# Kernel optimization log

Measured on AMD Instinct MI355X. Metric: run time of the kernel, lower is better.

## Reference

```python
import jax, jax.numpy as jnp
import numpy as np

B, C, H, W = 4, 96, 64, 64
D_STATE, D_CONV, EXPAND = 16, 4, 2
D_INNER = EXPAND * C          # 192
DT_RANK = (C + 15) // 16      # 6
BN_EPS = 1e-5


def setup_inputs() -> dict:
    key = jax.random.key(0)
    ks = jax.random.split(key, 10)
    s = 0.02
    return {
        "x": jax.random.normal(ks[0], (B, C, H, W), jnp.float32),
        # Mamba block params (mamba_ssm layout, no bias on in/out proj)
        "in_proj_w": jax.random.normal(ks[1], (2 * D_INNER, C), jnp.float32) * s,
        "conv1d_w": jax.random.normal(ks[2], (D_INNER, 1, D_CONV), jnp.float32) * s,  # depthwise
        "conv1d_b": jnp.zeros((D_INNER,), jnp.float32),
        "x_proj_w": jax.random.normal(ks[3], (DT_RANK + 2 * D_STATE, D_INNER), jnp.float32) * s,
        "dt_proj_w": jax.random.normal(ks[4], (D_INNER, DT_RANK), jnp.float32) * s,
        "dt_proj_b": jax.random.normal(ks[5], (D_INNER,), jnp.float32) * s,
        "A_log": jnp.log(jnp.tile(jnp.arange(1, D_STATE + 1, dtype=jnp.float32), (D_INNER, 1))),
        "D": jnp.ones((D_INNER,), jnp.float32),
        "out_proj_w": jax.random.normal(ks[6], (C, D_INNER), jnp.float32) * s,
        # trailing ConvBNReLU6 params
        "conv2d_w": jax.random.normal(ks[7], (C, C, 3, 3), jnp.float32) * s,
        "bn_gamma": jnp.ones((C,), jnp.float32),
        "bn_beta": jnp.zeros((C,), jnp.float32),
        "bn_mean": jnp.zeros((C,), jnp.float32),
        "bn_var": jnp.ones((C,), jnp.float32),
    }


def _forward(x, in_proj_w, conv1d_w, conv1d_b, x_proj_w, dt_proj_w, dt_proj_b,
             A_log, D, out_proj_w, conv2d_w, bn_gamma, bn_beta, bn_mean, bn_var):
    b, c, h, w = x.shape
    L = h * w
    seq = x.reshape(b, c, L).transpose(0, 2, 1)              # [B, L, C] tokens
    xz = seq @ in_proj_w.T                                    # [B, L, 2*D_INNER]
    xi, z = jnp.split(xz, 2, axis=-1)

    # depthwise causal conv1d + SiLU
    xi_c = jax.lax.conv_general_dilated(
        xi.transpose(0, 2, 1), conv1d_w, (1,), [(D_CONV - 1, 0)],
        dimension_numbers=("NCH", "OIH", "NCH"), feature_group_count=D_INNER)
    xi = jax.nn.silu((xi_c + conv1d_b[None, :, None]).transpose(0, 2, 1))  # [B, L, D_INNER]

    # input-dependent dt, B, C
    x_dbl = xi @ x_proj_w.T                                   # [B, L, DT_RANK + 2*D_STATE]
    dt, Bm, Cm = jnp.split(x_dbl, [DT_RANK, DT_RANK + D_STATE], axis=-1)
    dt = jax.nn.softplus(dt @ dt_proj_w.T + dt_proj_b)        # [B, L, D_INNER]

    # discretize: dA = exp(dt*A), dBx = dt*B*x
    A = -jnp.exp(A_log)                                       # [D_INNER, D_STATE]
    dA = jnp.exp(dt[..., None] * A)                           # [B, L, D_INNER, D_STATE]
    dBx = dt[..., None] * Bm[:, :, None, :] * xi[..., None]   # [B, L, D_INNER, D_STATE]

    def step(hst, inputs):
        dA_t, dBx_t, C_t = inputs
        hst = dA_t * hst + dBx_t                              # [B, D_INNER, D_STATE]
        y_t = jnp.einsum("bds,bs->bd", hst, C_t)
        return hst, y_t

    h0 = jnp.zeros((b, D_INNER, D_STATE), xi.dtype)
    _, ys = jax.lax.scan(step, h0,
                         (dA.transpose(1, 0, 2, 3), dBx.transpose(1, 0, 2, 3), Cm.transpose(1, 0, 2)))
    y = ys.transpose(1, 0, 2)                                 # [B, L, D_INNER]
    y = (y + xi * D) * jax.nn.silu(z)                         # skip D + gate
    out = y @ out_proj_w.T                                    # [B, L, C]
    xm = out.transpose(0, 2, 1).reshape(b, c, h, w)

    # ConvBNReLU: 3x3 conv (pad 1, no bias) -> BN (inference) -> ReLU6
    xo = jax.lax.conv_general_dilated(xm, conv2d_w, (1, 1), [(1, 1), (1, 1)],
                                      dimension_numbers=("NCHW", "OIHW", "NCHW"))
    inv = bn_gamma / jnp.sqrt(bn_var + BN_EPS)
    xo = xo * inv[None, :, None, None] + (bn_beta - bn_mean * inv)[None, :, None, None]
    return jnp.clip(xo, 0.0, 6.0)


def reference(x, in_proj_w, conv1d_w, conv1d_b, x_proj_w, dt_proj_w, dt_proj_b,
              A_log, D, out_proj_w, conv2d_w, bn_gamma, bn_beta, bn_mean, bn_var):
    return _forward(x, in_proj_w, conv1d_w, conv1d_b, x_proj_w, dt_proj_w, dt_proj_b,
                    A_log, D, out_proj_w, conv2d_w, bn_gamma, bn_beta, bn_mean, bn_var)
```

## Files before the change

### kernel.cpp

```cpp
#include <hip/hip_runtime.h>
#include <math.h>

#define LQ 4096
#define DI 192
#define DS 16
#define NCHUNK 64

__device__ __forceinline__ float siluf_(float v) { return v / (1.f + __expf(-v)); }
__device__ __forceinline__ float softplusf_(float v) { return v > 20.f ? v : log1pf(__expf(v)); }

template <int CTRL>
__device__ __forceinline__ float dpp_add16_(float x) {
    int y = __builtin_amdgcn_update_dpp(0, __float_as_int(x), CTRL, 0xf, 0xf, true);
    return x + __int_as_float(y);
}
template <int CTRL>
__device__ __forceinline__ float dpp_shift_(float x) {
    int y = __builtin_amdgcn_update_dpp(0, __float_as_int(x), CTRL, 0xf, 0xf, true);
    return __int_as_float(y);
}
__device__ __forceinline__ void async_g2l16_(const float* g, float* l) {
    __builtin_amdgcn_global_load_lds(
        (const __attribute__((address_space(1))) void*)g,
        (__attribute__((address_space(3))) void*)l, 16, 0, 0);
}
__device__ __forceinline__ void async_g2l4_(const float* g, float* l) {
    __builtin_amdgcn_global_load_lds(
        (const __attribute__((address_space(1))) void*)g,
        (__attribute__((address_space(3))) void*)l, 4, 0, 0);
}

__global__ __launch_bounds__(256) void k1_inproj(const float* __restrict__ x,
    const float* __restrict__ w, float* __restrict__ xi_raw, float* __restrict__ z)
{
    const int l0 = blockIdx.x * 64;
    const int n0 = blockIdx.y * 64;
    const int b  = blockIdx.z;
    __shared__ float xs[96 * 64];
    __shared__ float wsT[96 * 68];
    const int tid = threadIdx.x;
    for (int i = tid; i < 96 * 16; i += 256) {
        int c = i >> 4, lq = i & 15;
        *(float4*)&xs[c * 64 + lq * 4] =
            *(const float4*)&x[(b * 96 + c) * LQ + l0 + lq * 4];
    }
    for (int i = tid; i < 64 * 24; i += 256) {
        int n = i / 24, cq = i - n * 24;
        float4 v = *(const float4*)&w[(n0 + n) * 96 + cq * 4];
        wsT[(cq * 4 + 0) * 68 + n] = v.x;
        wsT[(cq * 4 + 1) * 68 + n] = v.y;
        wsT[(cq * 4 + 2) * 68 + n] = v.z;
        wsT[(cq * 4 + 3) * 68 + n] = v.w;
    }
    __syncthreads();
    const int tx = tid & 15;
    const int ty = tid >> 4;
    float acc[4][4];
#pragma unroll
    for (int i = 0; i < 4; ++i)
#pragma unroll
        for (int j = 0; j < 4; ++j) acc[i][j] = 0.f;
    for (int k = 0; k < 96; ++k) {
        float4 a  = *(const float4*)&xs[k * 64 + ty * 4];
        float4 bb = *(const float4*)&wsT[k * 68 + tx * 4];
        float av[4] = {a.x, a.y, a.z, a.w};
        float bv[4] = {bb.x, bb.y, bb.z, bb.w};
#pragma unroll
        for (int i = 0; i < 4; ++i)
#pragma unroll
            for (int j = 0; j < 4; ++j) acc[i][j] += av[i] * bv[j];
    }
    float* dst = (n0 < DI) ? xi_raw : z;
    const int nn0 = (n0 < DI) ? n0 : (n0 - DI);
#pragma unroll
    for (int i = 0; i < 4; ++i) {
        int l = l0 + ty * 4 + i;
        float4 v = make_float4(acc[i][0], acc[i][1], acc[i][2], acc[i][3]);
        *(float4*)&dst[(b * LQ + l) * DI + nn0 + tx * 4] = v;
    }
}

__global__ __launch_bounds__(256) void k2_conv1d(const float* __restrict__ xir,
    const float* __restrict__ cw, const float* __restrict__ cb, float* __restrict__ xi)
{
    int idx = blockIdx.x * 256 + threadIdx.x;
    int d = idx % DI;
    int l = (idx / DI) & (LQ - 1);
    float4 wv = *(const float4*)&cw[d * 4];
    float wk[4] = {wv.x, wv.y, wv.z, wv.w};
    float acc = cb[d];
#pragma unroll
    for (int k = 0; k < 4; ++k) {
        int lp = l - 3 + k;
        if (lp >= 0) acc += wk[k] * xir[idx + (k - 3) * DI];
    }
    xi[idx] = siluf_(acc);
}

__global__ __launch_bounds__(256) void k3_xdbl(const float* __restrict__ xi,
    const float* __restrict__ xw, float* __restrict__ xdbl)
{
    const int l0 = blockIdx.x * 64;
    const int b  = blockIdx.y;
    __shared__ float sxiT[96 * 68];
    __shared__ float swx[38 * 196];
    const int tid = threadIdx.x;
    for (int i = tid; i < 38 * 48; i += 256) {
        int n = i / 48, kq = i - n * 48;
        *(float4*)&swx[n * 196 + kq * 4] = *(const float4*)&xw[n * 192 + kq * 4];
    }
    const int lq = tid & 15, ng = tid >> 4;
    float acc[3][4];
#pragma unroll
    for (int p = 0; p < 3; ++p)
#pragma unroll
        for (int i = 0; i < 4; ++i) acc[p][i] = 0.f;
    for (int half = 0; half < 2; ++half) {
        __syncthreads();
        for (int i = tid; i < 64 * 24; i += 256) {
            int l = i / 24, kq = i - l * 24;
            float4 v = *(const float4*)&xi[(b * LQ + l0 + l) * DI + half * 96 + kq * 4];
            sxiT[(kq * 4 + 0) * 68 + l] = v.x;
            sxiT[(kq * 4 + 1) * 68 + l] = v.y;
            sxiT[(kq * 4 + 2) * 68 + l] = v.z;
            sxiT[(kq * 4 + 3) * 68 + l] = v.w;
        }
        __syncthreads();
#pragma unroll
        for (int pass = 0; pass < 3; ++pass) {
            int n = pass * 16 + ng;
            if (n >= 38) continue;
            for (int k = 0; k < 96; ++k) {
                float4 a = *(const float4*)&sxiT[k * 68 + lq * 4];
                float bv = swx[n * 196 + half * 96 + k];
                acc[pass][0] += a.x * bv;
                acc[pass][1] += a.y * bv;
                acc[pass][2] += a.z * bv;
                acc[pass][3] += a.w * bv;
            }
        }
    }
#pragma unroll
    for (int pass = 0; pass < 3; ++pass) {
        int n = pass * 16 + ng;
        if (n >= 38) continue;
#pragma unroll
        for (int i = 0; i < 4; ++i)
            xdbl[(b * LQ + l0 + lq * 4 + i) * 38 + n] = acc[pass][i];
    }
}

__global__ __launch_bounds__(256) void k4_scanA(
    const float* __restrict__ xdbl, const float* __restrict__ xi,
    const float* __restrict__ dtw, const float* __restrict__ dtb,
    const float* __restrict__ alog,
    float* __restrict__ cA, float* __restrict__ cB)
{
    const int ch = blockIdx.x, g = blockIdx.y, b = blockIdx.z;
    const int t0 = ch * 64, d0 = g * 16;
    __shared__ float sxd[64 * 40];
    __shared__ float sdt[1024], sxi[1024];
    __shared__ float sdtw[96], sdtb[16];
    const int tid = threadIdx.x;
    for (int i = tid; i < 64 * 38; i += 256) {
        int t = i / 38, cc = i - t * 38;
        sxd[t * 40 + cc] = xdbl[(b * LQ + t0 + t) * 38 + cc];
    }
    for (int i = tid; i < 1024; i += 256) {
        int t = i >> 4, j = i & 15;
        sxi[i] = xi[(b * LQ + t0 + t) * DI + d0 + j];
    }
    if (tid < 96) sdtw[tid] = dtw[d0 * 6 + tid];
    if (tid < 16) sdtb[tid] = dtb[d0 + tid];
    __syncthreads();
    for (int i = tid; i < 1024; i += 256) {
        int t = i >> 4, dl = i & 15;
        float acc = sdtb[dl];
#pragma unroll
        for (int r = 0; r < 6; ++r) acc += sxd[t * 40 + r] * sdtw[dl * 6 + r];
        sdt[i] = softplusf_(acc);
    }
    __syncthreads();
    const int s = tid & 15, dl = tid >> 4;
    const float Ads = -__expf(alog[(d0 + dl) * DS + s]);
    float a = 1.f, hb = 0.f;
#pragma unroll 4
    for (int t = 0; t < 64; ++t) {
        float dtv = sdt[t * 16 + dl];
        float dA = __expf(dtv * Ads);
        float dbx = dtv * sxd[t * 40 + 6 + s] * sxi[t * 16 + dl];
        a *= dA;
        hb = dA * hb + dbx;
    }
    int o = ((b * NCHUNK + ch) * DI + d0 + dl) * DS + s;
    cA[o] = a;
    cB[o] = hb;
}

__global__ __launch_bounds__(256) void k5_combine(const float* __restrict__ cA,
    const float* __restrict__ cB, float* __restrict__ hinit)
{
    int gid = blockIdx.x * 256 + threadIdx.x;
    int b = gid / 3072;
    int rem = gid - b * 3072;
    int base = b * (NCHUNK * 3072) + rem;
    float h = 0.f;
#pragma unroll 8
    for (int c = 0; c < NCHUNK; ++c) {
        int o = base + c * 3072;
        hinit[o] = h;
        h = cA[o] * h + cB[o];
    }
}

__global__ __launch_bounds__(256) void k6_scanC(
    const float* __restrict__ xdbl, const float* __restrict__ xi,
    const float* __restrict__ z, const float* __restrict__ dtw,
    const float* __restrict__ dtb, const float* __restrict__ alog,
    const float* __restrict__ Dp, const float* __restrict__ hinit,
    float* __restrict__ yg)
{
    const int ch = blockIdx.x, g = blockIdx.y, b = blockIdx.z;
    const int t0 = ch * 64, d0 = g * 16;
    __shared__ float sxd[64 * 40];
    __shared__ float sdt[1024], sxi[1024], szs[1024], sy[1024];
    __shared__ float sdtw[96], sdtb[16];
    const int tid = threadIdx.x;
    for (int i = tid; i < 64 * 38; i += 256) {
        int t = i / 38, cc = i - t * 38;
        sxd[t * 40 + cc] = xdbl[(b * LQ + t0 + t) * 38 + cc];
    }
    for (int i = tid; i < 1024; i += 256) {
        int t = i >> 4, j = i & 15;
        int row = b * LQ + t0 + t;
        sxi[i] = xi[row * DI + d0 + j];
        szs[i] = z[row * DI + d0 + j];
    }
    if (tid < 96) sdtw[tid] = dtw[d0 * 6 + tid];
    if (tid < 16) sdtb[tid] = dtb[d0 + tid];
    __syncthreads();
    for (int i = tid; i < 1024; i += 256) {
        int t = i >> 4, dl = i & 15;
        float acc = sdtb[dl];
#pragma unroll
        for (int r = 0; r < 6; ++r) acc += sxd[t * 40 + r] * sdtw[dl * 6 + r];
        sdt[i] = softplusf_(acc);
    }
    __syncthreads();
    const int s = tid & 15, dl = tid >> 4;
    const float Ads = -__expf(alog[(d0 + dl) * DS + s]);
    float h = hinit[((b * NCHUNK + ch) * DI + d0 + dl) * DS + s];
    for (int t = 0; t < 64; ++t) {
        float dtv = sdt[t * 16 + dl];
        float dA = __expf(dtv * Ads);
        h = dA * h + dtv * sxd[t * 40 + 6 + s] * sxi[t * 16 + dl];
        float p = h * sxd[t * 40 + 22 + s];
        p = dpp_add16_<0x128>(p);
        p = dpp_add16_<0x124>(p);
        p = dpp_add16_<0x122>(p);
        p = dpp_add16_<0x121>(p);
        if (s == 0) sy[t * 16 + dl] = p;
    }
    __syncthreads();
    for (int i = tid; i < 1024; i += 256) {
        int t = i >> 4, j = i & 15;
        float gate = siluf_(szs[i]);
        yg[(b * LQ + t0 + t) * DI + d0 + j] = (sy[i] + sxi[i] * Dp[d0 + j]) * gate;
    }
}

__global__ __launch_bounds__(256) void k7_outproj(const float* __restrict__ yg,
    const float* __restrict__ wo, float* __restrict__ xm)
{
    const int l0 = blockIdx.x * 64;
    const int n0 = blockIdx.y * 32;
    const int b  = blockIdx.z;
    __shared__ float syT[96 * 68];
    __shared__ float wtT[192 * 36];
    const int tid = threadIdx.x;
    for (int i = tid; i < 32 * 48; i += 256) {
        int n = i / 48, kq = i - n * 48;
        float4 v = *(const float4*)&wo[(n0 + n) * DI + kq * 4];
        wtT[(kq * 4 + 0) * 36 + n] = v.x;
        wtT[(kq * 4 + 1) * 36 + n] = v.y;
        wtT[(kq * 4 + 2) * 36 + n] = v.z;
        wtT[(kq * 4 + 3) * 36 + n] = v.w;
    }
    const int tx = tid & 15;
    const int ty = tid >> 4;
    float acc[2][4];
#pragma unroll
    for (int j = 0; j < 2; ++j)
#pragma unroll
        for (int i = 0; i < 4; ++i) acc[j][i] = 0.f;
    for (int half = 0; half < 2; ++half) {
        __syncthreads();
        for (int i = tid; i < 64 * 24; i += 256) {
            int l = i / 24, kq = i - l * 24;
            float4 v = *(const float4*)&yg[(b * LQ + l0 + l) * DI + half * 96 + kq * 4];
            syT[(kq * 4 + 0) * 68 + l] = v.x;
            syT[(kq * 4 + 1) * 68 + l] = v.y;
            syT[(kq * 4 + 2) * 68 + l] = v.z;
            syT[(kq * 4 + 3) * 68 + l] = v.w;
        }
        __syncthreads();
        for (int k = 0; k < 96; ++k) {
            float4 a = *(const float4*)&syT[k * 68 + tx * 4];
            int kk = half * 96 + k;
            float b0 = wtT[kk * 36 + ty * 2 + 0];
            float b1 = wtT[kk * 36 + ty * 2 + 1];
            acc[0][0] += a.x * b0; acc[0][1] += a.y * b0;
            acc[0][2] += a.z * b0; acc[0][3] += a.w * b0;
            acc[1][0] += a.x * b1; acc[1][1] += a.y * b1;
            acc[1][2] += a.z * b1; acc[1][3] += a.w * b1;
        }
    }
#pragma unroll
    for (int j = 0; j < 2; ++j) {
        float4 v = make_float4(acc[j][0], acc[j][1], acc[j][2], acc[j][3]);
        *(float4*)&xm[(b * 96 + n0 + ty * 2 + j) * LQ + l0 + tx * 4] = v;
    }
}

#define K8_INQ 384
#define K8_WNEL 576
__global__ __launch_bounds__(256) void k8_conv3(const float* __restrict__ xm,
    const float* __restrict__ w2, float* __restrict__ pbuf)
{
    const int ks  = blockIdx.x & 3;
    const int co0 = (blockIdx.x >> 2) * 16;
    const int y0  = blockIdx.y * 4;
    const int b   = blockIdx.z;
    __shared__ float sin2[2][1536];
    __shared__ float swt2[2][576];
    const int tid = threadIdx.x;
    const int sx = tid & 15;
    const int sy = (tid >> 4) & 3;
    const int cq = tid >> 6;

    int in_goff[2];
    bool in_ok[2];
#pragma unroll
    for (int j = 0; j < 2; ++j) {
        int i = tid + j * 256;
        int ci  = i / 96;
        int rem = i - ci * 96;
        int row = rem >> 4;
        int qx  = rem & 15;
        int gy  = y0 + row - 1;
        bool ok = (i < K8_INQ) && gy >= 0 && gy < 64;
        in_ok[j]  = ok;
        in_goff[j] = ok ? (ci * 4096 + gy * 64 + qx * 4) : 0;
    }
    int w_goff[3];
#pragma unroll
    for (int j = 0; j < 3; ++j) {
        int i = tid + j * 256;
        int ci  = i / 144;
        int rem = i - ci * 144;
        int k   = rem >> 4;
        int cl  = rem & 15;
        w_goff[j] = (i < K8_WNEL) ? (cl * 864 + ci * 9 + k) : 0;
    }

    const float* xb = xm + (size_t)b * 96 * 4096 + (size_t)ks * 24 * 4096;
    const float* wb = w2 + (size_t)co0 * 864 + ks * 24 * 9;
    const float4 zero4 = make_float4(0.f, 0.f, 0.f, 0.f);

#pragma unroll
    for (int bu = 0; bu < 2; ++bu) {
        if (!in_ok[0]) *(float4*)&sin2[bu][tid * 4] = zero4;
        if (tid < 128 && !in_ok[1]) *(float4*)&sin2[bu][(256 + tid) * 4] = zero4;
    }

    {
        const float* gx = xb;
        const float* gw = wb;
        if (in_ok[0]) async_g2l16_(gx + in_goff[0], &sin2[0][cq * 256]);
        if (tid < 128 && in_ok[1]) async_g2l16_(gx + in_goff[1], &sin2[0][1024 + cq * 256]);
        async_g2l4_(gw + w_goff[0], &swt2[0][cq * 64]);
        async_g2l4_(gw + w_goff[1], &swt2[0][256 + cq * 64]);
        if (tid < 64) async_g2l4_(gw + w_goff[2], &swt2[0][512 + cq * 64]);
    }
    __syncthreads();

    float acc[4][4];
#pragma unroll
    for (int c = 0; c < 4; ++c)
#pragma unroll
        for (int x = 0; x < 4; ++x) acc[c][x] = 0.f;

#pragma clang loop unroll(disable)
    for (int ch = 0; ch < 6; ++ch) {
        if (ch < 5) {
            const int nb = (ch + 1) & 1;
            const float* gx = xb + (ch + 1) * 16384;
            const float* gw = wb + (ch + 1) * 36;
            if (in_ok[0]) async_g2l16_(gx + in_goff[0], &sin2[nb][cq * 256]);
            if (tid < 128 && in_ok[1]) async_g2l16_(gx + in_goff[1], &sin2[nb][1024 + cq * 256]);
            async_g2l4_(gw + w_goff[0], &swt2[nb][cq * 64]);
            async_g2l4_(gw + w_goff[1], &swt2[nb][256 + cq * 64]);
            if (tid < 64) async_g2l4_(gw + w_goff[2], &swt2[nb][512 + cq * 64]);
        }

        const float* sc = sin2[ch & 1];
        const float* wc = swt2[ch & 1];
#pragma unroll
        for (int cii = 0; cii < 4; ++cii) {
            float w6[3][6];
#pragma unroll
            for (int r = 0; r < 3; ++r) {
                float4 v = *(const float4*)&sc[(cii * 6 + sy + r) * 64 + sx * 4];
                w6[r][0] = dpp_shift_<0x111>(v.w);
                w6[r][1] = v.x; w6[r][2] = v.y; w6[r][3] = v.z; w6[r][4] = v.w;
                w6[r][5] = dpp_shift_<0x101>(v.x);
            }
#pragma unroll
            for (int ky = 0; ky < 3; ++ky) {
#pragma unroll
                for (int kx = 0; kx < 3; ++kx) {
                    float4 wv = *(const float4*)&wc[(cii * 9 + ky * 3 + kx) * 16 + cq * 4];
#pragma unroll
                    for (int x = 0; x < 4; ++x) {
                        float pv = w6[ky][x + kx];
                        acc[0][x] = fmaf(pv, wv.x, acc[0][x]);
                        acc[1][x] = fmaf(pv, wv.y, acc[1][x]);
                        acc[2][x] = fmaf(pv, wv.z, acc[2][x]);
                        acc[3][x] = fmaf(pv, wv.w, acc[3][x]);
                    }
                }
            }
        }

        __syncthreads();
    }

    const int yy = y0 + sy;
    float* pb = pbuf + (size_t)ks * 1572864;
#pragma unroll
    for (int c = 0; c < 4; ++c) {
        const int cc = co0 + cq * 4 + c;
        float4 o = make_float4(acc[c][0], acc[c][1], acc[c][2], acc[c][3]);
        *(float4*)&pb[((size_t)(b * 96 + cc) * 64 + yy) * 64 + sx * 4] = o;
    }
}

__global__ __launch_bounds__(256) void k9_reduce(const float* __restrict__ pbuf,
    const float* __restrict__ bng, const float* __restrict__ bnb,
    const float* __restrict__ bnm, const float* __restrict__ bnv,
    float* __restrict__ out)
{
    const int q = blockIdx.x * 256 + threadIdx.x;
    const int idx = q * 4;
    const int c = (idx >> 12) % 96;
    float4 s = *(const float4*)&pbuf[idx];
    float4 s1 = *(const float4*)&pbuf[idx + 1572864];
    float4 s2 = *(const float4*)&pbuf[idx + 2 * 1572864];
    float4 s3 = *(const float4*)&pbuf[idx + 3 * 1572864];
    s.x += s1.x + s2.x + s3.x;
    s.y += s1.y + s2.y + s3.y;
    s.z += s1.z + s2.z + s3.z;
    s.w += s1.w + s2.w + s3.w;
    float inv = bng[c] / sqrtf(bnv[c] + 1e-5f);
    float add = bnb[c] - bnm[c] * inv;
    float4 o;
    o.x = fminf(fmaxf(s.x * inv + add, 0.f), 6.f);
    o.y = fminf(fmaxf(s.y * inv + add, 0.f), 6.f);
    o.z = fminf(fmaxf(s.z * inv + add, 0.f), 6.f);
    o.w = fminf(fmaxf(s.w * inv + add, 0.f), 6.f);
    *(float4*)&out[idx] = o;
}

extern "C" void kernel_launch(void* const* d_in, const int* in_sizes, int n_in,
                              void* d_out, int out_size, void* d_ws, size_t ws_size,
                              hipStream_t stream) {
    (void)in_sizes; (void)n_in; (void)out_size; (void)ws_size;
    const float* x    = (const float*)d_in[0];
    const float* w_in = (const float*)d_in[1];
    const float* cw   = (const float*)d_in[2];
    const float* cb   = (const float*)d_in[3];
    const float* xw   = (const float*)d_in[4];
    const float* dtw  = (const float*)d_in[5];
    const float* dtb  = (const float*)d_in[6];
    const float* alog = (const float*)d_in[7];
    const float* Dp   = (const float*)d_in[8];
    const float* wo   = (const float*)d_in[9];
    const float* w2   = (const float*)d_in[10];
    const float* bng  = (const float*)d_in[11];
    const float* bnb  = (const float*)d_in[12];
    const float* bnm  = (const float*)d_in[13];
    const float* bnv  = (const float*)d_in[14];

    float* ws = (float*)d_ws;
    float* xi_raw = ws;
    float* z      = ws + 3145728;
    float* xi     = ws + 6291456;
    float* xdbl   = ws + 9437184;
    float* cA     = ws + 10059776;
    float* cB     = ws + 10846208;
    float* hinit  = ws + 11632640;
    float* xm     = ws + 12419072;
    float* yg     = xi_raw;
    float* pbuf   = xi_raw;

    dim3 blk(256);
    k1_inproj<<<dim3(64, 6, 4), blk, 0, stream>>>(x, w_in, xi_raw, z);
    k2_conv1d<<<dim3(12288), blk, 0, stream>>>(xi_raw, cw, cb, xi);
    k3_xdbl<<<dim3(64, 4), blk, 0, stream>>>(xi, xw, xdbl);
    k4_scanA<<<dim3(NCHUNK, 12, 4), blk, 0, stream>>>(xdbl, xi, dtw, dtb, alog, cA, cB);
    k5_combine<<<dim3(48), blk, 0, stream>>>(cA, cB, hinit);
    k6_scanC<<<dim3(NCHUNK, 12, 4), blk, 0, stream>>>(xdbl, xi, z, dtw, dtb, alog, Dp, hinit, yg);
    k7_outproj<<<dim3(64, 3, 4), blk, 0, stream>>>(yg, wo, xm);
    k8_conv3<<<dim3(24, 16, 4), blk, 0, stream>>>(xm, w2, pbuf);
    k9_reduce<<<dim3(1536), blk, 0, stream>>>(pbuf, bng, bnb, bnm, bnv, (float*)d_out);
}
```

Measured before the change: 274.5 us.

## Drop split-K in 3x3 conv and fuse BN+ReLU6 epilogue, removing reduce kernel

The 3x3 conv previously split input channels four ways into a partial buffer, and a separate kernel summed the partials and applied BN and ReLU6. Each block now loops over all 96 input channels for 8 output channels and applies BN/ReLU6 directly before writing the output. This removes the partial-buffer write/read traffic and one kernel launch. In exchange the grid shrinks to 768 blocks, each with a longer serial loop and half the per-thread accumulators, so there is less parallelism and less register-level reuse of the input taps.

Result: no change. 275.9 us (+0.5%).

```diff
diff --git a/kernel.cpp b/kernel.cpp
--- a/kernel.cpp
+++ b/kernel.cpp
@@ -323,16 +323,17 @@
 }
 
 #define K8_INQ 384
-#define K8_WNEL 576
+#define K8_WNEL 288
 __global__ __launch_bounds__(256) void k8_conv3(const float* __restrict__ xm,
-    const float* __restrict__ w2, float* __restrict__ pbuf)
-{
-    const int ks  = blockIdx.x & 3;
-    const int co0 = (blockIdx.x >> 2) * 16;
+    const float* __restrict__ w2, const float* __restrict__ bng,
+    const float* __restrict__ bnb, const float* __restrict__ bnm,
+    const float* __restrict__ bnv, float* __restrict__ out)
+{
+    const int co0 = blockIdx.x * 8;
     const int y0  = blockIdx.y * 4;
     const int b   = blockIdx.z;
     __shared__ float sin2[2][1536];
-    __shared__ float swt2[2][576];
+    __shared__ float swt2[2][288];
     const int tid = threadIdx.x;
     const int sx = tid & 15;
     const int sy = (tid >> 4) & 3;
@@ -352,19 +353,19 @@
         in_ok[j]  = ok;
         in_goff[j] = ok ? (ci * 4096 + gy * 64 + qx * 4) : 0;
     }
-    int w_goff[3];
-#pragma unroll
-    for (int j = 0; j < 3; ++j) {
+    int w_goff[2];
+#pragma unroll
+    for (int j = 0; j < 2; ++j) {
         int i = tid + j * 256;
-        int ci  = i / 144;
-        int rem = i - ci * 144;
-        int k   = rem >> 4;
-        int cl  = rem & 15;
+        int ci  = i / 72;
+        int rem = i - ci * 72;
+        int k   = rem >> 3;
+        int cl  = rem & 7;
         w_goff[j] = (i < K8_WNEL) ? (cl * 864 + ci * 9 + k) : 0;
     }
 
-    const float* xb = xm + (size_t)b * 96 * 4096 + (size_t)ks * 24 * 4096;
-    const float* wb = w2 + (size_t)co0 * 864 + ks * 24 * 9;
+    const float* xb = xm + (size_t)b * 96 * 4096;
+    const float* wb = w2 + (size_t)co0 * 864;
     const float4 zero4 = make_float4(0.f, 0.f, 0.f, 0.f);
 
 #pragma unroll
@@ -374,33 +375,29 @@
     }
 
     {
-        const float* gx = xb;
-        const float* gw = wb;
-        if (in_ok[0]) async_g2l16_(gx + in_goff[0], &sin2[0][cq * 256]);
-        if (tid < 128 && in_ok[1]) async_g2l16_(gx + in_goff[1], &sin2[0][1024 + cq * 256]);
-        async_g2l4_(gw + w_goff[0], &swt2[0][cq * 64]);
-        async_g2l4_(gw + w_goff[1], &swt2[0][256 + cq * 64]);
-        if (tid < 64) async_g2l4_(gw + w_goff[2], &swt2[0][512 + cq * 64]);
-    }
-    __syncthreads();
-
-    float acc[4][4];
-#pragma unroll
-    for (int c = 0; c < 4; ++c)
+        if (in_ok[0]) async_g2l16_(xb + in_goff[0], &sin2[0][cq * 256]);
+        if (tid < 128 && in_ok[1]) async_g2l16_(xb + in_goff[1], &sin2[0][1024 + cq * 256]);
+        async_g2l4_(wb + w_goff[0], &swt2[0][cq * 64]);
+        if (tid < 32) async_g2l4_(wb + w_goff[1], &swt2[0][256]);
+    }
+    __syncthreads();
+
+    float acc[2][4];
+#pragma unroll
+    for (int c = 0; c < 2; ++c)
 #pragma unroll
         for (int x = 0; x < 4; ++x) acc[c][x] = 0.f;
 
 #pragma clang loop unroll(disable)
-    for (int ch = 0; ch < 6; ++ch) {
-        if (ch < 5) {
+    for (int ch = 0; ch < 24; ++ch) {
+        if (ch < 23) {
             const int nb = (ch + 1) & 1;
             const float* gx = xb + (ch + 1) * 16384;
             const float* gw = wb + (ch + 1) * 36;
             if (in_ok[0]) async_g2l16_(gx + in_goff[0], &sin2[nb][cq * 256]);
             if (tid < 128 && in_ok[1]) async_g2l16_(gx + in_goff[1], &sin2[nb][1024 + cq * 256]);
             async_g2l4_(gw + w_goff[0], &swt2[nb][cq * 64]);
-            async_g2l4_(gw + w_goff[1], &swt2[nb][256 + cq * 64]);
-            if (tid < 64) async_g2l4_(gw + w_goff[2], &swt2[nb][512 + cq * 64]);
+            if (tid < 32) async_g2l4_(gw + w_goff[1], &swt2[nb][256]);
         }
 
         const float* sc = sin2[ch & 1];
@@ -419,14 +416,12 @@
             for (int ky = 0; ky < 3; ++ky) {
 #pragma unroll
                 for (int kx = 0; kx < 3; ++kx) {
-                    float4 wv = *(const float4*)&wc[(cii * 9 + ky * 3 + kx) * 16 + cq * 4];
+                    float2 wv = *(const float2*)&wc[(cii * 9 + ky * 3 + kx) * 8 + cq * 2];
 #pragma unroll
                     for (int x = 0; x < 4; ++x) {
                         float pv = w6[ky][x + kx];
                         acc[0][x] = fmaf(pv, wv.x, acc[0][x]);
                         acc[1][x] = fmaf(pv, wv.y, acc[1][x]);
-                        acc[2][x] = fmaf(pv, wv.z, acc[2][x]);
-                        acc[3][x] = fmaf(pv, wv.w, acc[3][x]);
                     }
                 }
             }
@@ -436,39 +431,18 @@
     }
 
     const int yy = y0 + sy;
-    float* pb = pbuf + (size_t)ks * 1572864;
-#pragma unroll
-    for (int c = 0; c < 4; ++c) {
-        const int cc = co0 + cq * 4 + c;
-        float4 o = make_float4(acc[c][0], acc[c][1], acc[c][2], acc[c][3]);
-        *(float4*)&pb[((size_t)(b * 96 + cc) * 64 + yy) * 64 + sx * 4] = o;
-    }
-}
-
-__global__ __launch_bounds__(256) void k9_reduce(const float* __restrict__ pbuf,
-    const float* __restrict__ bng, const float* __restrict__ bnb,
-    const float* __restrict__ bnm, const float* __restrict__ bnv,
-    float* __restrict__ out)
-{
-    const int q = blockIdx.x * 256 + threadIdx.x;
-    const int idx = q * 4;
-    const int c = (idx >> 12) % 96;
-    float4 s = *(const float4*)&pbuf[idx];
-    float4 s1 = *(const float4*)&pbuf[idx + 1572864];
-    float4 s2 = *(const float4*)&pbuf[idx + 2 * 1572864];
-    float4 s3 = *(const float4*)&pbuf[idx + 3 * 1572864];
-    s.x += s1.x + s2.x + s3.x;
-    s.y += s1.y + s2.y + s3.y;
-    s.z += s1.z + s2.z + s3.z;
-    s.w += s1.w + s2.w + s3.w;
-    float inv = bng[c] / sqrtf(bnv[c] + 1e-5f);
-    float add = bnb[c] - bnm[c] * inv;
-    float4 o;
-    o.x = fminf(fmaxf(s.x * inv + add, 0.f), 6.f);
-    o.y = fminf(fmaxf(s.y * inv + add, 0.f), 6.f);
-    o.z = fminf(fmaxf(s.z * inv + add, 0.f), 6.f);
-    o.w = fminf(fmaxf(s.w * inv + add, 0.f), 6.f);
-    *(float4*)&out[idx] = o;
+#pragma unroll
+    for (int j = 0; j < 2; ++j) {
+        const int cc = co0 + cq * 2 + j;
+        float inv = bng[cc] / sqrtf(bnv[cc] + 1e-5f);
+        float add = bnb[cc] - bnm[cc] * inv;
+        float4 o;
+        o.x = fminf(fmaxf(acc[j][0] * inv + add, 0.f), 6.f);
+        o.y = fminf(fmaxf(acc[j][1] * inv + add, 0.f), 6.f);
+        o.z = fminf(fmaxf(acc[j][2] * inv + add, 0.f), 6.f);
+        o.w = fminf(fmaxf(acc[j][3] * inv + add, 0.f), 6.f);
+        *(float4*)&out[((size_t)(b * 96 + cc) * 64 + yy) * 64 + sx * 4] = o;
+    }
 }
 
 extern "C" void kernel_launch(void* const* d_in, const int* in_sizes, int n_in,
@@ -501,7 +475,6 @@
     float* hinit  = ws + 11632640;
     float* xm     = ws + 12419072;
     float* yg     = xi_raw;
-    float* pbuf   = xi_raw;
 
     dim3 blk(256);
     k1_inproj<<<dim3(64, 6, 4), blk, 0, stream>>>(x, w_in, xi_raw, z);
@@ -511,6 +484,5 @@
     k5_combine<<<dim3(48), blk, 0, stream>>>(cA, cB, hinit);
     k6_scanC<<<dim3(NCHUNK, 12, 4), blk, 0, stream>>>(xdbl, xi, z, dtw, dtb, alog, Dp, hinit, yg);
     k7_outproj<<<dim3(64, 3, 4), blk, 0, stream>>>(yg, wo, xm);
-    k8_conv3<<<dim3(24, 16, 4), blk, 0, stream>>>(xm, w2, pbuf);
-    k9_reduce<<<dim3(1536), blk, 0, stream>>>(pbuf, bng, bnb, bnm, bnv, (float*)d_out);
-}
+    k8_conv3<<<dim3(12, 16, 4), blk, 0, stream>>>(xm, w2, bng, bnb, bnm, bnv, (float*)d_out);
+}
```
